# Kernel optimization log

Hardware: AMD Instinct MI355X
Metric: run time of the kernel (lower is better)

The kernel has to match this reference:

```python
import jax, jax.numpy as jnp
import numpy as np

N, E, D, H, R = 50000, 800000, 128, 256, 4
P = 0.1  # node-drop probability (bernoulli(p)==1 -> node zeroed)


def setup_inputs() -> dict:
    key = jax.random.key(0)
    ks = jax.random.split(key, 5)
    x = jax.random.normal(ks[0], (N, D), jnp.float32)
    edge_index = jax.random.randint(ks[1], (2, E), 0, N)
    drop_mask = jax.random.bernoulli(ks[2], P, (R, N))  # True -> dropped
    W1 = jax.random.normal(ks[3], (D, H), jnp.float32) / np.sqrt(D)
    b1 = jnp.zeros((H,), jnp.float32)
    W2 = jax.random.normal(ks[4], (H, D), jnp.float32) / np.sqrt(H)
    b2 = jnp.zeros((D,), jnp.float32)
    return {"x": x, "edge_index": edge_index, "drop_mask": drop_mask,
            "W1": W1, "b1": b1, "W2": W2, "b2": b2}


def _mish(v):
    return v * jnp.tanh(jax.nn.softplus(v))


def reference(x, edge_index, drop_mask, W1, b1, W2, b2):
    src, dst = edge_index[0], edge_index[1]
    # multi-run node dropout: zero out dropped node rows per run  [R, N, D]
    x_runs = jnp.where(drop_mask[:, :, None], jnp.zeros((), x.dtype), x[None])
    # GIN aggregation per run: sum of source-node features at each target node
    agg = jax.vmap(lambda xr: jax.ops.segment_sum(xr[src], dst, num_segments=N))(x_runs)
    h = x_runs + agg  # (1 + eps) * x + aggr, eps = 0 (PyG GINConv default)
    out = _mish(h @ W1 + b1) @ W2 + b2  # [R, N, D]
    # mean over runs + residual with the ORIGINAL (un-dropped) x
    return out.mean(axis=0) + x
```

## Files before the change

### kernel.cpp

```cpp
#include <hip/hip_runtime.h>
#include <cstdint>
#include <cstddef>

#define NN 50000
#define NE 800000
#define DF 128
#define HF 256
#define NR 4
#define NB1 196

typedef __attribute__((ext_vector_type(8))) short short8;
typedef __attribute__((ext_vector_type(4))) float f32x4;
typedef __attribute__((ext_vector_type(4))) unsigned short ushort4v;

static const size_t H_BYTES = (size_t)NR * NN * DF * 2;
static const size_t W1T_OFF = H_BYTES;
static const size_t W2T_OFF = W1T_OFF + (size_t)DF * HF * 2;
static const size_t INT_OFF = W2T_OFF + (size_t)DF * HF * 2;

__device__ __forceinline__ unsigned short f2bf(float f) {
  union { float f; unsigned u; } v; v.f = f;
  unsigned r = v.u + 0x7FFF + ((v.u >> 16) & 1);
  return (unsigned short)(r >> 16);
}

__device__ __forceinline__ float mishf(float z) {
  float t = __expf(z);
  float u = fmaf(t, t + 2.f, 1.f);
  float m = z * (u - 1.f) / (u + 1.f);
  return (z > 30.f) ? z : m;
}

__global__ __launch_bounds__(256) void k_zero_deg(int* __restrict__ deg, int* __restrict__ flag) {
  int n = blockIdx.x * 256 + threadIdx.x;
  if (n < NN) deg[n] = 0;
  if (n == 0) *flag = 0;
}

__global__ __launch_bounds__(256) void k_detect(const unsigned char* __restrict__ dropb,
                                                int* __restrict__ flag) {
  int i = blockIdx.x * 256 + threadIdx.x;
  if (i < NR * NN && (i & 3) != 0 && dropb[i] != 0) atomicOr(flag, 1);
}

__global__ __launch_bounds__(256) void k_pack(const unsigned char* __restrict__ dropb,
                                              const int* __restrict__ dropi,
                                              const int* __restrict__ flag,
                                              unsigned char* __restrict__ bits) {
  int n = blockIdx.x * 256 + threadIdx.x;
  if (n < NN) {
    const int byte_mode = *flag;
    unsigned b = 0;
#pragma unroll
    for (int r = 0; r < NR; ++r) {
      int v = byte_mode ? (int)dropb[(size_t)r * NN + n] : dropi[(size_t)r * NN + n];
      b |= (v != 0 ? 1u : 0u) << r;
    }
    bits[n] = (unsigned char)b;
  }
}

__global__ __launch_bounds__(256) void k_hist(const int* __restrict__ ei, int* __restrict__ deg) {
  int e = blockIdx.x * 256 + threadIdx.x;
  if (e < NE) atomicAdd(&deg[ei[NE + e]], 1);
}

__global__ __launch_bounds__(256) void k_scan1(const int* __restrict__ deg,
    int* __restrict__ rowstart, int* __restrict__ bsum) {
  __shared__ int s[256];
  int t = threadIdx.x, n = blockIdx.x * 256 + t;
  int v = (n < NN) ? deg[n] : 0;
  s[t] = v; __syncthreads();
  for (int off = 1; off < 256; off <<= 1) {
    int a = s[t]; int b = (t >= off) ? s[t - off] : 0;
    __syncthreads(); s[t] = a + b; __syncthreads();
  }
  if (n < NN) rowstart[n] = s[t] - v;
  if (t == 255) bsum[blockIdx.x] = s[255];
}

__global__ __launch_bounds__(256) void k_scan2(const int* __restrict__ bsum, int* __restrict__ boff) {
  __shared__ int s[256];
  int t = threadIdx.x;
  int v = (t < NB1) ? bsum[t] : 0;
  s[t] = v; __syncthreads();
  for (int off = 1; off < 256; off <<= 1) {
    int a = s[t]; int b = (t >= off) ? s[t - off] : 0;
    __syncthreads(); s[t] = a + b; __syncthreads();
  }
  if (t < NB1) boff[t] = s[t] - v;
}

__global__ __launch_bounds__(256) void k_scan3(int* __restrict__ rowstart,
    const int* __restrict__ boff, int* __restrict__ cursor) {
  int n = blockIdx.x * 256 + threadIdx.x;
  if (n < NN) {
    int rs = rowstart[n] + boff[blockIdx.x];
    rowstart[n] = rs;
    cursor[n] = rs;
  }
}

__global__ __launch_bounds__(256) void k_fill(const int* __restrict__ ei,
    int* __restrict__ cursor, int* __restrict__ adj) {
  int e = blockIdx.x * 256 + threadIdx.x;
  if (e < NE) {
    int src = ei[e], dst = ei[NE + e];
    int pos = atomicAdd(&cursor[dst], 1);
    adj[pos] = src;
  }
}

__global__ __launch_bounds__(256) void k_wprep(const float* __restrict__ W1,
    const float* __restrict__ W2, unsigned short* __restrict__ W1T,
    unsigned short* __restrict__ W2T) {
  int i = blockIdx.x * 256 + threadIdx.x;
  if (i < DF * HF) {
    int n = i >> 7, k = i & 127;
    W1T[i] = f2bf(W1[(size_t)k * HF + n]);
  } else {
    int j = i - DF * HF;
    int n = j >> 8, k = j & 255;
    W2T[j] = f2bf(W2[(size_t)k * DF + n]);
  }
}

__global__ __launch_bounds__(256) void k_gather(const float* __restrict__ x,
    const int* __restrict__ adj, const int* __restrict__ rowstart,
    const int* __restrict__ deg, const unsigned char* __restrict__ bits,
    unsigned short* __restrict__ H) {
  const int n  = blockIdx.x * 8 + (threadIdx.x >> 5);
  const int d4 = (threadIdx.x & 31) * 4;
  const int start = rowstart[n], dg = deg[n];
  float4 aS = make_float4(0.f, 0.f, 0.f, 0.f);
  float4 aC[NR];
#pragma unroll
  for (int r = 0; r < NR; ++r) aC[r] = make_float4(0.f, 0.f, 0.f, 0.f);

  int i = 0;
  for (; i + 2 <= dg; i += 2) {
    int s0 = adj[start + i], s1 = adj[start + i + 1];
    const float4 v0 = *(const float4*)&x[(size_t)s0 * DF + d4];
    const float4 v1 = *(const float4*)&x[(size_t)s1 * DF + d4];
    unsigned b0 = bits[s0], b1 = bits[s1];
    aS.x += v0.x + v1.x; aS.y += v0.y + v1.y;
    aS.z += v0.z + v1.z; aS.w += v0.w + v1.w;
#pragma unroll
    for (int r = 0; r < NR; ++r) {
      if (b0 & (1u << r)) { aC[r].x += v0.x; aC[r].y += v0.y; aC[r].z += v0.z; aC[r].w += v0.w; }
      if (b1 & (1u << r)) { aC[r].x += v1.x; aC[r].y += v1.y; aC[r].z += v1.z; aC[r].w += v1.w; }
    }
  }
  if (i < dg) {
    int s0 = adj[start + i];
    const float4 v0 = *(const float4*)&x[(size_t)s0 * DF + d4];
    unsigned b0 = bits[s0];
    aS.x += v0.x; aS.y += v0.y; aS.z += v0.z; aS.w += v0.w;
#pragma unroll
    for (int r = 0; r < NR; ++r)
      if (b0 & (1u << r)) { aC[r].x += v0.x; aC[r].y += v0.y; aC[r].z += v0.z; aC[r].w += v0.w; }
  }

  const float4 x4 = *(const float4*)&x[(size_t)n * DF + d4];
  const unsigned bn = bits[n];
#pragma unroll
  for (int r = 0; r < NR; ++r) {
    float hx = aS.x - aC[r].x, hy = aS.y - aC[r].y;
    float hz = aS.z - aC[r].z, hw = aS.w - aC[r].w;
    if (!((bn >> r) & 1)) { hx += x4.x; hy += x4.y; hz += x4.z; hw += x4.w; }
    ushort4v u;
    u.x = f2bf(hx); u.y = f2bf(hy); u.z = f2bf(hz); u.w = f2bf(hw);
    *(ushort4v*)&H[((size_t)(n * NR + r)) * DF + d4] = u;
  }
}

__global__ __launch_bounds__(256) void k_mlp_mfma(const unsigned short* __restrict__ H,
    const unsigned short* __restrict__ W1T, const unsigned short* __restrict__ W2T,
    const float* __restrict__ b1, const float* __restrict__ b2,
    const float* __restrict__ x, float* __restrict__ out) {
  __shared__ unsigned char lds[49152];
  unsigned char* HsB = lds;
  unsigned char* AsB = lds + 16384;

  const int tid = threadIdx.x;
  const int wid = tid >> 6, lane = tid & 63;
  const int lg = lane >> 4, lr = lane & 15;
  const int row0 = blockIdx.x * 64;
  const int swz = (lr & 7) << 4;

  const unsigned char* Hsrc = (const unsigned char*)(H + (size_t)row0 * DF);
#pragma unroll
  for (int c = 0; c < 4; ++c) {
    int q = tid * 4 + c;
    int row = q >> 4, kb = (q & 15) * 16;
    short8 v = *(const short8*)(Hsrc + (size_t)q * 16);
    *(short8*)(HsB + row * 256 + (kb ^ ((row & 7) << 4))) = v;
  }
  __syncthreads();

  f32x4 acc1[4][4] = {};
#pragma unroll
  for (int ks = 0; ks < 4; ++ks) {
    short8 Af[4];
#pragma unroll
    for (int m = 0; m < 4; ++m)
      Af[m] = *(const short8*)(HsB + (m * 16 + lr) * 256 + ((ks * 64 + lg * 16) ^ swz));
#pragma unroll
    for (int nr = 0; nr < 4; ++nr) {
      int n1 = wid * 64 + nr * 16 + lr;
      short8 Bf = *(const short8*)(W1T + (size_t)n1 * DF + ks * 32 + lg * 8);
#pragma unroll
      for (int m = 0; m < 4; ++m)
        acc1[m][nr] = __builtin_amdgcn_mfma_f32_16x16x32_bf16(Af[m], Bf, acc1[m][nr], 0, 0, 0);
    }
  }

#pragma unroll
  for (int nr = 0; nr < 4; ++nr) {
    int col = wid * 64 + nr * 16 + lr;
    float bb = b1[col];
#pragma unroll
    for (int m = 0; m < 4; ++m) {
#pragma unroll
      for (int i = 0; i < 4; ++i) {
        int row = m * 16 + lg * 4 + i;
        float a = mishf(acc1[m][nr][i] + bb);
        *(unsigned short*)(AsB + row * 512 + ((col * 2) ^ ((row & 7) << 4))) = f2bf(a);
      }
    }
  }
  __syncthreads();

  f32x4 acc2[4][2] = {};
#pragma unroll
  for (int ks = 0; ks < 8; ++ks) {
    short8 Af[4];
#pragma unroll
    for (int m = 0; m < 4; ++m)
      Af[m] = *(const short8*)(AsB + (m * 16 + lr) * 512 + ((ks * 64 + lg * 16) ^ swz));
#pragma unroll
    for (int nr = 0; nr < 2; ++nr) {
      int n2 = wid * 32 + nr * 16 + lr;
      short8 Bf = *(const short8*)(W2T + (size_t)n2 * HF + ks * 32 + lg * 8);
#pragma unroll
      for (int m = 0; m < 4; ++m)
        acc2[m][nr] = __builtin_amdgcn_mfma_f32_16x16x32_bf16(Af[m], Bf, acc2[m][nr], 0, 0, 0);
    }
  }

  const int nodebase = row0 >> 2;
#pragma unroll
  for (int m = 0; m < 4; ++m) {
    int node = nodebase + m * 4 + lg;
#pragma unroll
    for (int nr = 0; nr < 2; ++nr) {
      int col = wid * 32 + nr * 16 + lr;
      float mean = 0.25f * (acc2[m][nr][0] + acc2[m][nr][1] + acc2[m][nr][2] + acc2[m][nr][3]);
      out[(size_t)node * DF + col] = mean + b2[col] + x[(size_t)node * DF + col];
    }
  }
}

extern "C" void kernel_launch(void* const* d_in, const int* in_sizes, int n_in,
                              void* d_out, int out_size, void* d_ws, size_t ws_size,
                              hipStream_t stream) {
  const float* x             = (const float*)d_in[0];
  const int* ei              = (const int*)d_in[1];
  const unsigned char* dropb = (const unsigned char*)d_in[2];
  const int* dropi           = (const int*)d_in[2];
  const float* W1            = (const float*)d_in[3];
  const float* b1            = (const float*)d_in[4];
  const float* W2            = (const float*)d_in[5];
  const float* b2            = (const float*)d_in[6];
  float* out = (float*)d_out;

  unsigned char* wsb = (unsigned char*)d_ws;
  unsigned short* H   = (unsigned short*)wsb;
  unsigned short* W1T = (unsigned short*)(wsb + W1T_OFF);
  unsigned short* W2T = (unsigned short*)(wsb + W2T_OFF);
  int* deg      = (int*)(wsb + INT_OFF);
  int* rowstart = deg + NN;
  int* cursor   = rowstart + NN;
  int* bsum     = cursor + NN;
  int* boff     = bsum + 256;
  int* adj      = boff + 256;
  int* flag     = adj + NE;
  unsigned char* bits = (unsigned char*)(flag + 1);

  k_zero_deg<<<NB1, 256, 0, stream>>>(deg, flag);
  k_detect<<<(NR * NN + 255) / 256, 256, 0, stream>>>(dropb, flag);
  k_pack<<<NB1, 256, 0, stream>>>(dropb, dropi, flag, bits);
  k_hist<<<(NE + 255) / 256, 256, 0, stream>>>(ei, deg);
  k_scan1<<<NB1, 256, 0, stream>>>(deg, rowstart, bsum);
  k_scan2<<<1, 256, 0, stream>>>(bsum, boff);
  k_scan3<<<NB1, 256, 0, stream>>>(rowstart, boff, cursor);
  k_fill<<<(NE + 255) / 256, 256, 0, stream>>>(ei, cursor, adj);
  k_wprep<<<(2 * DF * HF) / 256, 256, 0, stream>>>(W1, W2, W1T, W2T);
  k_gather<<<NN / 8, 256, 0, stream>>>(x, adj, rowstart, deg, bits, H);
  k_mlp_mfma<<<(NR * NN) / 64, 256, 0, stream>>>(H, W1T, W2T, b1, b2, x, out);
}
```

Baseline: 315.8 us.

## Fuse gather into MLP kernel, merge setup kernels, single-block scan

The neighbour gather now builds the bf16 H tile directly in LDS inside the MFMA MLP kernel, which removes the global H round trip of about 51MB write plus read. Several small setup kernels are merged: weight prep with zeroing, and pack with histogram. The three-pass scan is replaced by a single 1024-thread block scan. Mish now uses a reciprocal and packed bf16 conversion, and the first GEMM is transposed so the epilogue can do vector LDS stores. The trade-off is that the serial single-block scan and the fused kernel's lower occupancy could hide gather latency less well.

```diff
diff --git a/kernel.cpp b/kernel.cpp
--- a/kernel.cpp
+++ b/kernel.cpp
@@ -7,16 +7,13 @@
 #define DF 128
 #define HF 256
 #define NR 4
-#define NB1 196
 
 typedef __attribute__((ext_vector_type(8))) short short8;
 typedef __attribute__((ext_vector_type(4))) float f32x4;
-typedef __attribute__((ext_vector_type(4))) unsigned short ushort4v;
-
-static const size_t H_BYTES = (size_t)NR * NN * DF * 2;
-static const size_t W1T_OFF = H_BYTES;
-static const size_t W2T_OFF = W1T_OFF + (size_t)DF * HF * 2;
-static const size_t INT_OFF = W2T_OFF + (size_t)DF * HF * 2;
+
+static const size_t W1T_OFF = 0;
+static const size_t W2T_OFF = (size_t)DF * HF;
+static const size_t INT_OFF = W2T_OFF + (size_t)DF * HF;
 
 __device__ __forceinline__ unsigned short f2bf(float f) {
   union { float f; unsigned u; } v; v.f = f;
@@ -24,17 +21,31 @@
   return (unsigned short)(r >> 16);
 }
 
+__device__ __forceinline__ unsigned cvtpk(float a, float b) {
+  unsigned r;
+  asm("v_cvt_pk_bf16_f32 %0, %1, %2" : "=v"(r) : "v"(a), "v"(b));
+  return r;
+}
+
 __device__ __forceinline__ float mishf(float z) {
   float t = __expf(z);
   float u = fmaf(t, t + 2.f, 1.f);
-  float m = z * (u - 1.f) / (u + 1.f);
-  return (z > 30.f) ? z : m;
-}
-
-__global__ __launch_bounds__(256) void k_zero_deg(int* __restrict__ deg, int* __restrict__ flag) {
-  int n = blockIdx.x * 256 + threadIdx.x;
-  if (n < NN) deg[n] = 0;
-  if (n == 0) *flag = 0;
+  float r = __builtin_amdgcn_rcpf(u + 1.f);
+  return fmaf(-(z + z), r, z);
+}
+
+__global__ __launch_bounds__(256) void k_init(const float* __restrict__ W1,
+    const float* __restrict__ W2, unsigned short* __restrict__ W1T,
+    unsigned short* __restrict__ W2T, int* __restrict__ deg, int* __restrict__ flag) {
+  int i = blockIdx.x * 256 + threadIdx.x;
+  if (i < NN) deg[i] = 0;
+  if (i == 0) *flag = 0;
+  if (i < DF * HF) {
+    int n = i >> 7, k = i & 127;
+    W1T[i] = f2bf(W1[(size_t)k * HF + n]);
+    int n2 = i >> 8, k2 = i & 255;
+    W2T[i] = f2bf(W2[(size_t)k2 * DF + n2]);
+  }
 }
 
 __global__ __launch_bounds__(256) void k_detect(const unsigned char* __restrict__ dropb,
@@ -43,62 +54,37 @@
   if (i < NR * NN && (i & 3) != 0 && dropb[i] != 0) atomicOr(flag, 1);
 }
 
-__global__ __launch_bounds__(256) void k_pack(const unsigned char* __restrict__ dropb,
-                                              const int* __restrict__ dropi,
-                                              const int* __restrict__ flag,
-                                              unsigned char* __restrict__ bits) {
-  int n = blockIdx.x * 256 + threadIdx.x;
-  if (n < NN) {
+__global__ __launch_bounds__(256) void k_packhist(const unsigned char* __restrict__ dropb,
+    const int* __restrict__ dropi, const int* __restrict__ flag,
+    unsigned char* __restrict__ bits, const int* __restrict__ ei, int* __restrict__ deg) {
+  int t = blockIdx.x * 256 + threadIdx.x;
+  if (t < NE) atomicAdd(&deg[ei[NE + t]], 1);
+  if (t < NN) {
     const int byte_mode = *flag;
     unsigned b = 0;
 #pragma unroll
     for (int r = 0; r < NR; ++r) {
-      int v = byte_mode ? (int)dropb[(size_t)r * NN + n] : dropi[(size_t)r * NN + n];
+      int v = byte_mode ? (int)dropb[(size_t)r * NN + t] : dropi[(size_t)r * NN + t];
       b |= (v != 0 ? 1u : 0u) << r;
     }
-    bits[n] = (unsigned char)b;
-  }
-}
-
-__global__ __launch_bounds__(256) void k_hist(const int* __restrict__ ei, int* __restrict__ deg) {
-  int e = blockIdx.x * 256 + threadIdx.x;
-  if (e < NE) atomicAdd(&deg[ei[NE + e]], 1);
-}
-
-__global__ __launch_bounds__(256) void k_scan1(const int* __restrict__ deg,
-    int* __restrict__ rowstart, int* __restrict__ bsum) {
-  __shared__ int s[256];
-  int t = threadIdx.x, n = blockIdx.x * 256 + t;
-  int v = (n < NN) ? deg[n] : 0;
-  s[t] = v; __syncthreads();
-  for (int off = 1; off < 256; off <<= 1) {
+    bits[t] = (unsigned char)b;
+  }
+}
+
+__global__ __launch_bounds__(1024) void k_scan(const int* __restrict__ deg,
+    int* __restrict__ rowstart, int* __restrict__ cursor) {
+  __shared__ int s[1024];
+  const int t = threadIdx.x;
+  const int lo = t * 49, hi = (lo + 49 < NN) ? lo + 49 : NN;
+  int loc = 0;
+  for (int j = lo; j < hi; ++j) loc += deg[j];
+  s[t] = loc; __syncthreads();
+  for (int off = 1; off < 1024; off <<= 1) {
     int a = s[t]; int b = (t >= off) ? s[t - off] : 0;
     __syncthreads(); s[t] = a + b; __syncthreads();
   }
-  if (n < NN) rowstart[n] = s[t] - v;
-  if (t == 255) bsum[blockIdx.x] = s[255];
-}
-
-__global__ __launch_bounds__(256) void k_scan2(const int* __restrict__ bsum, int* __restrict__ boff) {
-  __shared__ int s[256];
-  int t = threadIdx.x;
-  int v = (t < NB1) ? bsum[t] : 0;
-  s[t] = v; __syncthreads();
-  for (int off = 1; off < 256; off <<= 1) {
-    int a = s[t]; int b = (t >= off) ? s[t - off] : 0;
-    __syncthreads(); s[t] = a + b; __syncthreads();
-  }
-  if (t < NB1) boff[t] = s[t] - v;
-}
-
-__global__ __launch_bounds__(256) void k_scan3(int* __restrict__ rowstart,
-    const int* __restrict__ boff, int* __restrict__ cursor) {
-  int n = blockIdx.x * 256 + threadIdx.x;
-  if (n < NN) {
-    int rs = rowstart[n] + boff[blockIdx.x];
-    rowstart[n] = rs;
-    cursor[n] = rs;
-  }
+  int run = s[t] - loc;
+  for (int j = lo; j < hi; ++j) { rowstart[j] = run; cursor[j] = run; run += deg[j]; }
 }
 
 __global__ __launch_bounds__(256) void k_fill(const int* __restrict__ ei,
@@ -111,122 +97,116 @@
   }
 }
 
-__global__ __launch_bounds__(256) void k_wprep(const float* __restrict__ W1,
-    const float* __restrict__ W2, unsigned short* __restrict__ W1T,
-    unsigned short* __restrict__ W2T) {
-  int i = blockIdx.x * 256 + threadIdx.x;
-  if (i < DF * HF) {
-    int n = i >> 7, k = i & 127;
-    W1T[i] = f2bf(W1[(size_t)k * HF + n]);
-  } else {
-    int j = i - DF * HF;
-    int n = j >> 8, k = j & 255;
-    W2T[j] = f2bf(W2[(size_t)k * DF + n]);
-  }
-}
-
-__global__ __launch_bounds__(256) void k_gather(const float* __restrict__ x,
+__global__ __launch_bounds__(256) void k_mlp(const float* __restrict__ x,
     const int* __restrict__ adj, const int* __restrict__ rowstart,
     const int* __restrict__ deg, const unsigned char* __restrict__ bits,
-    unsigned short* __restrict__ H) {
-  const int n  = blockIdx.x * 8 + (threadIdx.x >> 5);
-  const int d4 = (threadIdx.x & 31) * 4;
-  const int start = rowstart[n], dg = deg[n];
-  float4 aS = make_float4(0.f, 0.f, 0.f, 0.f);
-  float4 aC[NR];
-#pragma unroll
-  for (int r = 0; r < NR; ++r) aC[r] = make_float4(0.f, 0.f, 0.f, 0.f);
-
-  int i = 0;
-  for (; i + 2 <= dg; i += 2) {
-    int s0 = adj[start + i], s1 = adj[start + i + 1];
-    const float4 v0 = *(const float4*)&x[(size_t)s0 * DF + d4];
-    const float4 v1 = *(const float4*)&x[(size_t)s1 * DF + d4];
-    unsigned b0 = bits[s0], b1 = bits[s1];
-    aS.x += v0.x + v1.x; aS.y += v0.y + v1.y;
-    aS.z += v0.z + v1.z; aS.w += v0.w + v1.w;
-#pragma unroll
-    for (int r = 0; r < NR; ++r) {
-      if (b0 & (1u << r)) { aC[r].x += v0.x; aC[r].y += v0.y; aC[r].z += v0.z; aC[r].w += v0.w; }
-      if (b1 & (1u << r)) { aC[r].x += v1.x; aC[r].y += v1.y; aC[r].z += v1.z; aC[r].w += v1.w; }
-    }
-  }
-  if (i < dg) {
-    int s0 = adj[start + i];
-    const float4 v0 = *(const float4*)&x[(size_t)s0 * DF + d4];
-    unsigned b0 = bits[s0];
-    aS.x += v0.x; aS.y += v0.y; aS.z += v0.z; aS.w += v0.w;
-#pragma unroll
-    for (int r = 0; r < NR; ++r)
-      if (b0 & (1u << r)) { aC[r].x += v0.x; aC[r].y += v0.y; aC[r].z += v0.z; aC[r].w += v0.w; }
-  }
-
-  const float4 x4 = *(const float4*)&x[(size_t)n * DF + d4];
-  const unsigned bn = bits[n];
-#pragma unroll
-  for (int r = 0; r < NR; ++r) {
-    float hx = aS.x - aC[r].x, hy = aS.y - aC[r].y;
-    float hz = aS.z - aC[r].z, hw = aS.w - aC[r].w;
-    if (!((bn >> r) & 1)) { hx += x4.x; hy += x4.y; hz += x4.z; hw += x4.w; }
-    ushort4v u;
-    u.x = f2bf(hx); u.y = f2bf(hy); u.z = f2bf(hz); u.w = f2bf(hw);
-    *(ushort4v*)&H[((size_t)(n * NR + r)) * DF + d4] = u;
-  }
-}
-
-__global__ __launch_bounds__(256) void k_mlp_mfma(const unsigned short* __restrict__ H,
     const unsigned short* __restrict__ W1T, const unsigned short* __restrict__ W2T,
     const float* __restrict__ b1, const float* __restrict__ b2,
-    const float* __restrict__ x, float* __restrict__ out) {
-  __shared__ unsigned char lds[49152];
+    float* __restrict__ out) {
+  __shared__ __align__(16) unsigned char lds[49152];
   unsigned char* HsB = lds;
   unsigned char* AsB = lds + 16384;
 
   const int tid = threadIdx.x;
+
+  {
+    const int ln = tid >> 4, li = tid & 15;
+    const int n = blockIdx.x * 16 + ln;
+    const int d0 = li * 8;
+    const int start = rowstart[n], dg = deg[n];
+    float s[8] = {0, 0, 0, 0, 0, 0, 0, 0};
+    float c[NR][8] = {};
+
+    int i = 0;
+    for (; i + 2 <= dg; i += 2) {
+      int s0 = adj[start + i], s1 = adj[start + i + 1];
+      const float4 a0 = *(const float4*)&x[(size_t)s0 * DF + d0];
+      const float4 a1 = *(const float4*)&x[(size_t)s0 * DF + d0 + 4];
+      const float4 b0 = *(const float4*)&x[(size_t)s1 * DF + d0];
+      const float4 b1v = *(const float4*)&x[(size_t)s1 * DF + d0 + 4];
+      unsigned m0 = bits[s0], m1 = bits[s1];
+      s[0] += a0.x + b0.x; s[1] += a0.y + b0.y; s[2] += a0.z + b0.z; s[3] += a0.w + b0.w;
+      s[4] += a1.x + b1v.x; s[5] += a1.y + b1v.y; s[6] += a1.z + b1v.z; s[7] += a1.w + b1v.w;
+#pragma unroll
+      for (int r = 0; r < NR; ++r) {
+        if ((m0 >> r) & 1) {
+          c[r][0] += a0.x; c[r][1] += a0.y; c[r][2] += a0.z; c[r][3] += a0.w;
+          c[r][4] += a1.x; c[r][5] += a1.y; c[r][6] += a1.z; c[r][7] += a1.w;
+        }
+        if ((m1 >> r) & 1) {
+          c[r][0] += b0.x; c[r][1] += b0.y; c[r][2] += b0.z; c[r][3] += b0.w;
+          c[r][4] += b1v.x; c[r][5] += b1v.y; c[r][6] += b1v.z; c[r][7] += b1v.w;
+        }
+      }
+    }
+    if (i < dg) {
+      int s0 = adj[start + i];
+      const float4 a0 = *(const float4*)&x[(size_t)s0 * DF + d0];
+      const float4 a1 = *(const float4*)&x[(size_t)s0 * DF + d0 + 4];
+      unsigned m0 = bits[s0];
+      s[0] += a0.x; s[1] += a0.y; s[2] += a0.z; s[3] += a0.w;
+      s[4] += a1.x; s[5] += a1.y; s[6] += a1.z; s[7] += a1.w;
+#pragma unroll
+      for (int r = 0; r < NR; ++r)
+        if ((m0 >> r) & 1) {
+          c[r][0] += a0.x; c[r][1] += a0.y; c[r][2] += a0.z; c[r][3] += a0.w;
+          c[r][4] += a1.x; c[r][5] += a1.y; c[r][6] += a1.z; c[r][7] += a1.w;
+        }
+    }
+
+    const float4 x0 = *(const float4*)&x[(size_t)n * DF + d0];
+    const float4 x1 = *(const float4*)&x[(size_t)n * DF + d0 + 4];
+    const float xs[8] = {x0.x, x0.y, x0.z, x0.w, x1.x, x1.y, x1.z, x1.w};
+    const unsigned bn = bits[n];
+#pragma unroll
+    for (int r = 0; r < NR; ++r) {
+      float h[8];
+      const float keep = ((bn >> r) & 1) ? 0.f : 1.f;
+#pragma unroll
+      for (int j = 0; j < 8; ++j) h[j] = s[j] - c[r][j] + keep * xs[j];
+      uint4 p;
+      p.x = cvtpk(h[0], h[1]); p.y = cvtpk(h[2], h[3]);
+      p.z = cvtpk(h[4], h[5]); p.w = cvtpk(h[6], h[7]);
+      const int row = ln * 4 + r;
+      *(uint4*)(HsB + row * 256 + ((li * 16) ^ ((row & 7) << 4))) = p;
+    }
+  }
+  __syncthreads();
+
   const int wid = tid >> 6, lane = tid & 63;
   const int lg = lane >> 4, lr = lane & 15;
-  const int row0 = blockIdx.x * 64;
   const int swz = (lr & 7) << 4;
 
-  const unsigned char* Hsrc = (const unsigned char*)(H + (size_t)row0 * DF);
-#pragma unroll
-  for (int c = 0; c < 4; ++c) {
-    int q = tid * 4 + c;
-    int row = q >> 4, kb = (q & 15) * 16;
-    short8 v = *(const short8*)(Hsrc + (size_t)q * 16);
-    *(short8*)(HsB + row * 256 + (kb ^ ((row & 7) << 4))) = v;
-  }
-  __syncthreads();
-
   f32x4 acc1[4][4] = {};
 #pragma unroll
   for (int ks = 0; ks < 4; ++ks) {
-    short8 Af[4];
-#pragma unroll
-    for (int m = 0; m < 4; ++m)
-      Af[m] = *(const short8*)(HsB + (m * 16 + lr) * 256 + ((ks * 64 + lg * 16) ^ swz));
-#pragma unroll
-    for (int nr = 0; nr < 4; ++nr) {
-      int n1 = wid * 64 + nr * 16 + lr;
-      short8 Bf = *(const short8*)(W1T + (size_t)n1 * DF + ks * 32 + lg * 8);
-#pragma unroll
-      for (int m = 0; m < 4; ++m)
-        acc1[m][nr] = __builtin_amdgcn_mfma_f32_16x16x32_bf16(Af[m], Bf, acc1[m][nr], 0, 0, 0);
-    }
-  }
-
-#pragma unroll
-  for (int nr = 0; nr < 4; ++nr) {
-    int col = wid * 64 + nr * 16 + lr;
-    float bb = b1[col];
-#pragma unroll
-    for (int m = 0; m < 4; ++m) {
-#pragma unroll
-      for (int i = 0; i < 4; ++i) {
-        int row = m * 16 + lg * 4 + i;
-        float a = mishf(acc1[m][nr][i] + bb);
-        *(unsigned short*)(AsB + row * 512 + ((col * 2) ^ ((row & 7) << 4))) = f2bf(a);
-      }
+    short8 Bf[4];
+#pragma unroll
+    for (int rt = 0; rt < 4; ++rt)
+      Bf[rt] = *(const short8*)(HsB + (rt * 16 + lr) * 256 + ((ks * 64 + lg * 16) ^ swz));
+#pragma unroll
+    for (int ht = 0; ht < 4; ++ht) {
+      short8 Af = *(const short8*)(W1T + (size_t)(wid * 64 + ht * 16 + lr) * DF + ks * 32 + lg * 8);
+#pragma unroll
+      for (int rt = 0; rt < 4; ++rt)
+        acc1[ht][rt] = __builtin_amdgcn_mfma_f32_16x16x32_bf16(Af, Bf[rt], acc1[ht][rt], 0, 0, 0);
+    }
+  }
+
+#pragma unroll
+  for (int ht = 0; ht < 4; ++ht) {
+    const float4 bb = *(const float4*)&b1[wid * 64 + ht * 16 + lg * 4];
+    const int chunk = wid * 128 + ht * 32 + (lg >> 1) * 16;
+    const int sub = (lg & 1) * 8;
+#pragma unroll
+    for (int rt = 0; rt < 4; ++rt) {
+      const int row = rt * 16 + lr;
+      float m0 = mishf(acc1[ht][rt][0] + bb.x);
+      float m1 = mishf(acc1[ht][rt][1] + bb.y);
+      float m2 = mishf(acc1[ht][rt][2] + bb.z);
+      float m3 = mishf(acc1[ht][rt][3] + bb.w);
+      uint2 p; p.x = cvtpk(m0, m1); p.y = cvtpk(m2, m3);
+      *(uint2*)(AsB + row * 512 + (chunk ^ ((row & 7) << 4)) + sub) = p;
     }
   }
   __syncthreads();
@@ -240,21 +220,20 @@
       Af[m] = *(const short8*)(AsB + (m * 16 + lr) * 512 + ((ks * 64 + lg * 16) ^ swz));
 #pragma unroll
     for (int nr = 0; nr < 2; ++nr) {
-      int n2 = wid * 32 + nr * 16 + lr;
-      short8 Bf = *(const short8*)(W2T + (size_t)n2 * HF + ks * 32 + lg * 8);
+      short8 Bf = *(const short8*)(W2T + (size_t)(wid * 32 + nr * 16 + lr) * HF + ks * 32 + lg * 8);
 #pragma unroll
       for (int m = 0; m < 4; ++m)
         acc2[m][nr] = __builtin_amdgcn_mfma_f32_16x16x32_bf16(Af[m], Bf, acc2[m][nr], 0, 0, 0);
     }
   }
 
-  const int nodebase = row0 >> 2;
+  const int nodebase = blockIdx.x * 16;
 #pragma unroll
   for (int m = 0; m < 4; ++m) {
-    int node = nodebase + m * 4 + lg;
+    const int node = nodebase + m * 4 + lg;
 #pragma unroll
     for (int nr = 0; nr < 2; ++nr) {
-      int col = wid * 32 + nr * 16 + lr;
+      const int col = wid * 32 + nr * 16 + lr;
       float mean = 0.25f * (acc2[m][nr][0] + acc2[m][nr][1] + acc2[m][nr][2] + acc2[m][nr][3]);
       out[(size_t)node * DF + col] = mean + b2[col] + x[(size_t)node * DF + col];
     }
@@ -274,28 +253,20 @@
   const float* b2            = (const float*)d_in[6];
   float* out = (float*)d_out;
 
-  unsigned char* wsb = (unsigned char*)d_ws;
-  unsigned short* H   = (unsigned short*)wsb;
-  unsigned short* W1T = (unsigned short*)(wsb + W1T_OFF);
-  unsigned short* W2T = (unsigned short*)(wsb + W2T_OFF);
-  int* deg      = (int*)(wsb + INT_OFF);
+  unsigned short* wsh = (unsigned short*)d_ws;
+  unsigned short* W1T = wsh + W1T_OFF;
+  unsigned short* W2T = wsh + W2T_OFF;
+  int* deg      = (int*)(wsh + INT_OFF);
   int* rowstart = deg + NN;
   int* cursor   = rowstart + NN;
-  int* bsum     = cursor + NN;
-  int* boff     = bsum + 256;
-  int* adj      = boff + 256;
+  int* adj      = cursor + NN;
   int* flag     = adj + NE;
   unsigned char* bits = (unsigned char*)(flag + 1);
 
-  k_zero_deg<<<NB1, 256, 0, stream>>>(deg, flag);
+  k_init<<<256, 256, 0, stream>>>(W1, W2, W1T, W2T, deg, flag);
   k_detect<<<(NR * NN + 255) / 256, 256, 0, stream>>>(dropb, flag);
-  k_pack<<<NB1, 256, 0, stream>>>(dropb, dropi, flag, bits);
-  k_hist<<<(NE + 255) / 256, 256, 0, stream>>>(ei, deg);
-  k_scan1<<<NB1, 256, 0, stream>>>(deg, rowstart, bsum);
-  k_scan2<<<1, 256, 0, stream>>>(bsum, boff);
-  k_scan3<<<NB1, 256, 0, stream>>>(rowstart, boff, cursor);
+  k_packhist<<<(NE + 255) / 256, 256, 0, stream>>>(dropb, dropi, flag, bits, ei, deg);
+  k_scan<<<1, 1024, 0, stream>>>(deg, rowstart, cursor);
   k_fill<<<(NE + 255) / 256, 256, 0, stream>>>(ei, cursor, adj);
-  k_wprep<<<(2 * DF * HF) / 256, 256, 0, stream>>>(W1, W2, W1T, W2T);
-  k_gather<<<NN / 8, 256, 0, stream>>>(x, adj, rowstart, deg, bits, H);
-  k_mlp_mfma<<<(NR * NN) / 64, 256, 0, stream>>>(H, W1T, W2T, b1, b2, x, out);
-}
+  k_mlp<<<NN / 16, 256, 0, stream>>>(x, adj, rowstart, deg, bits, W1T, W2T, b1, b2, out);
+}
```

Result: slower. 424.9 us (+34.5%).
